# Optimization experiments

Measured on AMD Instinct MI355X. Metric: run time of the kernel, lower is better.

Reference implementation:

```python
import jax, jax.numpy as jnp
from jax import lax
import numpy as np

PI = np.float32(np.pi)
DN = ('NCHW', 'OIHW', 'NCHW')
PAD = [(1, 1), (1, 1)]


def setup_inputs() -> dict:
    key = jax.random.key(0)
    k1, k2 = jax.random.split(key, 2)
    B, C, H, W_ = 8, 64, 256, 256
    OUT, K = 64, 8
    x = jax.random.normal(k1, (B, C, H, W_), dtype=jnp.float32)
    # kaiming-normal-like scale for 3x3 conv weights
    W = jax.random.normal(k2, (K, OUT, C, 3, 3), dtype=jnp.float32) * np.float32(np.sqrt(2.0 / (C * 9)))
    b = jnp.zeros((K, OUT), dtype=jnp.float32)  # nn.init.zeros_(conv.bias)
    return {"x": x, "W": W, "b": b}


def reference(x, W, b):
    B, C, H, Wd = x.shape
    K = W.shape[0]
    sx = jnp.array([[1, 0, -1], [2, 0, -2], [1, 0, -1]], dtype=jnp.float32)
    sy = jnp.array([[1, 2, 1], [0, 0, 0], [-1, -2, -1]], dtype=jnp.float32)
    kx = jnp.tile(sx[None, None], (C, 1, 1, 1))  # (C,1,3,3) depthwise
    ky = jnp.tile(sy[None, None], (C, 1, 1, 1))
    grad_x = lax.conv_general_dilated(x, kx, (1, 1), PAD, dimension_numbers=DN, feature_group_count=C)
    grad_y = lax.conv_general_dilated(x, ky, (1, 1), PAD, dimension_numbers=DN, feature_group_count=C)
    theta = jnp.arctan2(grad_y, grad_x)
    # ((theta+pi)/(2pi)*K).long() % K ; values >= 0 so trunc == floor
    q = ((theta + PI) / (2 * PI) * K).astype(jnp.int32) % K  # (B,C,H,W)
    out = jnp.zeros((B, W.shape[1], H, Wd), dtype=x.dtype)
    for k in range(K):
        mask = (q == k).astype(x.dtype)
        fk = lax.conv_general_dilated(x * mask, W[k], (1, 1), PAD, dimension_numbers=DN)
        out = out + fk + b[k][None, :, None, None]
    return out / K
```

## Files before the change

kernel.cpp:

```cpp
#include <hip/hip_runtime.h>
#include <math.h>


#define TH 16
#define TW 32

typedef __attribute__((ext_vector_type(8)))  short    short8;
typedef __attribute__((ext_vector_type(16))) float    f32x16;
typedef __attribute__((ext_vector_type(4)))  unsigned u32x4;

__device__ __forceinline__ float atanf_fdlibm(float x) {
#pragma clang fp contract(off)
    const float atanhi0 = 4.6364760399e-01f, atanhi1 = 7.8539812565e-01f,
                atanhi2 = 9.8279368877e-01f, atanhi3 = 1.5707962513e+00f;
    const float atanlo0 = 5.0121582440e-09f, atanlo1 = 3.7748947079e-08f,
                atanlo2 = 3.4473217170e-08f, atanlo3 = 7.5497894159e-08f;
    const float aT0 = 3.3333334327e-01f, aT1 = -2.0000000298e-01f, aT2 = 1.4285714924e-01f,
                aT3 = -1.1111110449e-01f, aT4 = 9.0908870101e-02f, aT5 = -7.6918758452e-02f,
                aT6 = 6.6610731184e-02f, aT7 = -5.8335702866e-02f, aT8 = 4.9768779427e-02f,
                aT9 = -3.6531571299e-02f, aT10 = 1.6285819933e-02f;

    int hx = __float_as_int(x);
    int ix = hx & 0x7fffffff;
    int id;
    if (ix >= 0x4c800000) {
        if (ix > 0x7f800000) return x + x;
        return (hx > 0) ? (atanhi3 + atanlo3) : (-atanhi3 - atanlo3);
    }
    if (ix < 0x3ee00000) {
        if (ix < 0x31000000) return x;
        id = -1;
    } else {
        x = fabsf(x);
        if (ix < 0x3f980000) {
            if (ix < 0x3f300000) { id = 0; x = (2.0f * x - 1.0f) / (2.0f + x); }
            else                 { id = 1; x = (x - 1.0f) / (x + 1.0f); }
        } else {
            if (ix < 0x401c0000) { id = 2; x = (x - 1.5f) / (1.0f + 1.5f * x); }
            else                 { id = 3; x = -1.0f / x; }
        }
    }
    float z = x * x;
    float w = z * z;
    float s1 = z * (aT0 + w * (aT2 + w * (aT4 + w * (aT6 + w * (aT8 + w * aT10)))));
    float s2 = w * (aT1 + w * (aT3 + w * (aT5 + w * (aT7 + w * aT9))));
    if (id < 0) return x - x * (s1 + s2);
    float r;
    if      (id == 0) r = atanhi0 - ((x * (s1 + s2) - atanlo0) - x);
    else if (id == 1) r = atanhi1 - ((x * (s1 + s2) - atanlo1) - x);
    else if (id == 2) r = atanhi2 - ((x * (s1 + s2) - atanlo2) - x);
    else              r = atanhi3 - ((x * (s1 + s2) - atanlo3) - x);
    return (hx < 0) ? -r : r;
}

__device__ __forceinline__ float atan2f_fdlibm(float y, float x) {
#pragma clang fp contract(off)
    const float tiny = 1.0e-30f;
    const float pi_o_4 = 7.8539818525e-01f;
    const float pi_o_2 = 1.5707963705e+00f;
    const float pi     = 3.1415927410e+00f;
    const float pi_lo  = -8.7422776573e-08f;

    int hx = __float_as_int(x), hy = __float_as_int(y);
    int ix = hx & 0x7fffffff, iy = hy & 0x7fffffff;
    if (ix > 0x7f800000 || iy > 0x7f800000) return x + y;
    if (hx == 0x3f800000) return atanf_fdlibm(y);
    int m = ((hy >> 31) & 1) | ((hx >> 30) & 2);

    if (iy == 0) {
        switch (m) {
            case 0:
            case 1:  return y;
            case 2:  return  pi + tiny;
            default: return -pi - tiny;
        }
    }
    if (ix == 0) return (hy < 0) ? (-pi_o_2 - tiny) : (pi_o_2 + tiny);
    if (ix == 0x7f800000) {
        if (iy == 0x7f800000) {
            switch (m) {
                case 0:  return  pi_o_4 + tiny;
                case 1:  return -pi_o_4 - tiny;
                case 2:  return  3.0f * pi_o_4 + tiny;
                default: return -3.0f * pi_o_4 - tiny;
            }
        } else {
            switch (m) {
                case 0:  return  0.0f;
                case 1:  return -0.0f;
                case 2:  return  pi + tiny;
                default: return -pi - tiny;
            }
        }
    }
    if (iy == 0x7f800000) return (hy < 0) ? (-pi_o_2 - tiny) : (pi_o_2 + tiny);

    int k = (iy - ix) >> 23;
    float z;
    int mm = m;
    if (k > 26)                    { z = pi_o_2 + 0.5f * pi_lo; mm &= 1; }
    else if (hx < 0 && k < -26)    { z = 0.0f; }
    else                           { z = atanf_fdlibm(fabsf(y / x)); }

    switch (mm) {
        case 0:  return z;
        case 1:  return -z;
        case 2:  return pi - (z - pi_lo);
        default: return (z - pi_lo) - pi;
    }
}

__device__ __forceinline__ int bin8(float gy, float gx) {
#pragma clang fp contract(off)
    float th = atan2f_fdlibm(gy, gx);
    float t  = th + 3.14159274101257324f;
    float u  = t / 6.28318548202514648f;
    u = u * 8.0f;
    return ((int)u) & 7;
}

__device__ __forceinline__ unsigned rne_bf16_bits(float f) {
    unsigned u = __float_as_uint(f);
    return (u + 0x7fffu + ((u >> 16) & 1u)) >> 16;
}

__global__ __launch_bounds__(256)
void bin_kernel(const float* __restrict__ x, unsigned* __restrict__ pwg) {
    __shared__ float rs[3][260];
    const int w    = threadIdx.x;
    const int hrow = blockIdx.x;
    const int img  = blockIdx.y;
    const float* xim = x + ((size_t)img << 16);
    #pragma unroll
    for (int r = 0; r < 3; ++r) {
        int gh = hrow - 1 + r;
        float v = 0.f;
        if ((unsigned)gh < 256u) v = xim[(gh << 8) + w];
        rs[r][w + 1] = v;
        if (w == 0) { rs[r][0] = 0.f; rs[r][257] = 0.f; }
    }
    __syncthreads();
    int q; unsigned hv;
    {
#pragma clang fp contract(off)
        float a0 = rs[0][w], a1 = rs[0][w + 1], a2 = rs[0][w + 2];
        float m0 = rs[1][w],                    m2 = rs[1][w + 2];
        float z0 = rs[2][w], z1 = rs[2][w + 1], z2 = rs[2][w + 2];
        float gx = ((((a0 - a2) + 2.0f * m0) - 2.0f * m2) + z0) - z2;
        float gy = ((((a0 + 2.0f * a1) + a2) - z0) - 2.0f * z1) - z2;
        q  = bin8(gy, gx);
        hv = rne_bf16_bits(rs[1][w + 1]);
    }
    pwg[((size_t)img << 16) + (hrow << 8) + w] = (hv << 16) | (unsigned)q;
}

__global__ void prep_w2(const float* __restrict__ Wg, short* __restrict__ wsw) {
    int tid = blockIdx.x * 256 + threadIdx.x;
    if (tid >= 4096) return;
    int c = tid >> 6, o = tid & 63;
    for (int t = 0; t < 9; ++t)
        #pragma unroll
        for (int k = 0; k < 8; ++k)
            wsw[((((c * 10 + t) << 6) + o) << 3) + k] =
                (short)rne_bf16_bits(Wg[(((k << 6) + o) * 64 + c) * 9 + t]);
    #pragma unroll
    for (int k = 0; k < 8; ++k)
        wsw[((((c * 10 + 9) << 6) + o) << 3) + k] = 0;
}

__device__ __forceinline__ void build_oh(unsigned pv, u32x4* dst) {
    unsigned q  = pv & 7u;
    unsigned hv = (q & 1u) ? (pv & 0xffff0000u) : (pv >> 16);
    unsigned s2 = q >> 1;
    u32x4 oh;
    oh.x = (s2 == 0u) ? hv : 0u;
    oh.y = (s2 == 1u) ? hv : 0u;
    oh.z = (s2 == 2u) ? hv : 0u;
    oh.w = (s2 == 3u) ? hv : 0u;
    *dst = oh;
}

__global__ __launch_bounds__(256, 2)
void dirconv_mfma2(const unsigned* __restrict__ pwg,
                   const short*    __restrict__ wsw,
                   const float*    __restrict__ bg,
                   float*          __restrict__ out) {
    __shared__ u32x4 pwx[2][648];
    __shared__ u32x4 wl2[2][640];
    __shared__ float bsum[64];

    const int tid  = threadIdx.x;
    const int wave = tid >> 6;
    const int lane = tid & 63;
    const int h    = lane >> 5;
    const int l31  = lane & 31;
    const int bb   = blockIdx.z;
    const int h0   = blockIdx.y * TH;
    const int w0c  = blockIdx.x * TW;

    if (tid < 64) {
        float s = 0.f;
        #pragma unroll
        for (int k = 0; k < 8; ++k) s += bg[k * 64 + tid];
        bsum[tid] = s;
    }

    f32x16 acc[2][4];
    #pragma unroll
    for (int i = 0; i < 2; ++i)
        #pragma unroll
        for (int j = 0; j < 4; ++j)
            acc[i][j] = (f32x16)0.f;

    int rro[5], c2o[5];
    #pragma unroll
    for (int s = 0; s < 5; ++s) {
        int t = 2 * s + h;
        int t3 = t / 3;
        rro[s] = (t <= 8) ? t3 : 0;
        c2o[s] = (t <= 8) ? (t - t3 * 3) : 0;
    }

    {
        const u32x4* wsrc = (const u32x4*)wsw;
        wl2[0][tid]       = wsrc[tid];
        wl2[0][tid + 256] = wsrc[tid + 256];
        if (tid < 128) wl2[0][tid + 512] = wsrc[tid + 512];
        const unsigned* pimg = pwg + ((size_t)(bb * 64) << 16);
        #pragma unroll
        for (int rd = 0; rd < 3; ++rd) {
            int idx = tid + rd * 256;
            if (idx < 612) {
                int r = idx / 34, cc2 = idx - r * 34;
                int gh = h0 + r - 1, gw = w0c + cc2 - 1;
                unsigned pv = 0;
                if ((unsigned)gh < 256u && (unsigned)gw < 256u)
                    pv = pimg[(gh << 8) + gw];
                build_oh(pv, &pwx[0][r * 36 + cc2]);
            }
        }
    }
    __syncthreads();

    #pragma unroll 2
    for (int c = 0; c < 64; ++c) {
        const int cb = c & 1, nb = cb ^ 1;
        u32x4 wv0 = (u32x4)0u, wv1 = (u32x4)0u, wv2 = (u32x4)0u;
        unsigned pv0 = 0, pv1 = 0, pv2 = 0;

        if (c < 63) {
            const u32x4* wsrc = (const u32x4*)(wsw + (size_t)(c + 1) * 5120);
            wv0 = wsrc[tid];
            wv1 = wsrc[tid + 256];
            if (tid < 128) wv2 = wsrc[tid + 512];
            const unsigned* pimg = pwg + ((size_t)(bb * 64 + c + 1) << 16);
            {   int idx = tid;       int r = idx / 34, cc2 = idx - r * 34;
                int gh = h0 + r - 1, gw = w0c + cc2 - 1;
                if ((unsigned)gh < 256u && (unsigned)gw < 256u) pv0 = pimg[(gh << 8) + gw]; }
            {   int idx = tid + 256; int r = idx / 34, cc2 = idx - r * 34;
                int gh = h0 + r - 1, gw = w0c + cc2 - 1;
                if ((unsigned)gh < 256u && (unsigned)gw < 256u) pv1 = pimg[(gh << 8) + gw]; }
            if (tid < 100) {
                int idx = tid + 512; int r = idx / 34, cc2 = idx - r * 34;
                int gh = h0 + r - 1, gw = w0c + cc2 - 1;
                if ((unsigned)gh < 256u && (unsigned)gw < 256u) pv2 = pimg[(gh << 8) + gw]; }
        }

        {
            const u32x4* pb = &pwx[cb][0];
            const u32x4* wb = &wl2[cb][0];
            #pragma unroll
            for (int s = 0; s < 5; ++s) {
                const int t = 2 * s + h;
                short8 a0 = __builtin_bit_cast(short8, wb[t * 64 + l31]);
                short8 a1 = __builtin_bit_cast(short8, wb[t * 64 + 32 + l31]);
                #pragma unroll
                for (int nf = 0; nf < 4; ++nf) {
                    int py = wave * 4 + nf;
                    short8 bf = __builtin_bit_cast(short8,
                                    pb[(py + rro[s]) * 36 + l31 + c2o[s]]);
                    acc[0][nf] = __builtin_amdgcn_mfma_f32_32x32x16_bf16(a0, bf, acc[0][nf], 0, 0, 0);
                    acc[1][nf] = __builtin_amdgcn_mfma_f32_32x32x16_bf16(a1, bf, acc[1][nf], 0, 0, 0);
                }
            }
        }

        if (c < 63) {
            wl2[nb][tid]       = wv0;
            wl2[nb][tid + 256] = wv1;
            if (tid < 128) wl2[nb][tid + 512] = wv2;
            {   int idx = tid;       int r = idx / 34, cc2 = idx - r * 34;
                build_oh(pv0, &pwx[nb][r * 36 + cc2]); }
            {   int idx = tid + 256; int r = idx / 34, cc2 = idx - r * 34;
                build_oh(pv1, &pwx[nb][r * 36 + cc2]); }
            if (tid < 100) {
                int idx = tid + 512; int r = idx / 34, cc2 = idx - r * 34;
                build_oh(pv2, &pwx[nb][r * 36 + cc2]); }
        }
        __syncthreads();
    }

    float* ob = out + ((size_t)bb << 22);
    #pragma unroll
    for (int mf = 0; mf < 2; ++mf)
        #pragma unroll
        for (int nf = 0; nf < 4; ++nf) {
            int py = wave * 4 + nf;
            #pragma unroll
            for (int reg = 0; reg < 16; ++reg) {
                int o = mf * 32 + (reg & 3) + 8 * (reg >> 2) + 4 * h;
                ob[((size_t)o << 16) + ((h0 + py) << 8) + (w0c + l31)] =
                    (acc[mf][nf][reg] + bsum[o]) * 0.125f;
            }
        }
}

__global__ __launch_bounds__(256, 2)
void dirconv_fb(const float* __restrict__ x,
                const float* __restrict__ Wg,
                const float* __restrict__ bg,
                float* __restrict__ out) {
    __shared__ float    xs[20 * 37];
    __shared__ unsigned pw[18 * 36];
    __shared__ short    wl[64][128];
    __shared__ float    bsum[64];

    const int tid  = threadIdx.x;
    const int wave = tid >> 6;
    const int lane = tid & 63;
    const int h    = lane >> 5;
    const int l31  = lane & 31;
    const int bb   = blockIdx.z;
    const int h0   = blockIdx.y * TH;
    const int w0   = blockIdx.x * TW;

    if (tid < 64) {
        float s = 0.f;
        #pragma unroll
        for (int k = 0; k < 8; ++k) s += bg[k * 64 + tid];
        bsum[tid] = s;
    }

    f32x16 acc[2][4];
    #pragma unroll
    for (int i = 0; i < 2; ++i)
        #pragma unroll
        for (int j = 0; j < 4; ++j)
            acc[i][j] = (f32x16)0.f;

    const int swz0 = l31 & 7;

    for (int c = 0; c < 64; ++c) {
        __syncthreads();
        const float* xc = x + ((size_t)(bb * 64 + c) << 16);
        for (int idx = tid; idx < 720; idx += 256) {
            int r = idx / 36, cc = idx - r * 36;
            int gh = h0 + r - 2, gw = w0 + cc - 2;
            float v = 0.f;
            if ((unsigned)gh < 256u && (unsigned)gw < 256u)
                v = xc[(gh << 8) + gw];
            xs[r * 37 + cc] = v;
        }
        for (int pair = tid; pair < 512; pair += 256) {
            int k = pair >> 6, o = pair & 63;
            const float* g = Wg + ((size_t)((k << 6) + o) * 64 + c) * 9;
            #pragma unroll
            for (int t = 0; t < 9; ++t)
                wl[o][((t ^ (o & 7)) << 3) + k] = (short)rne_bf16_bits(g[t]);
        }
        if (tid < 64) {
            int o = tid;
            #pragma unroll
            for (int e = 0; e < 8; ++e) wl[o][((9 ^ (o & 7)) << 3) + e] = 0;
        }
        __syncthreads();

        for (int idx = tid; idx < 612; idx += 256) {
            int r = idx / 34, cc = idx - r * 34;
            const float* p0 = &xs[r * 37 + cc];
            int q; unsigned hv;
            {
#pragma clang fp contract(off)
                float a0 = p0[0],  a1 = p0[1],  a2 = p0[2];
                float m0 = p0[37],              m2 = p0[39];
                float z0 = p0[74], z1 = p0[75], z2 = p0[76];
                float gx = ((((a0 - a2) + 2.0f * m0) - 2.0f * m2) + z0) - z2;
                float gy = ((((a0 + 2.0f * a1) + a2) - z0) - 2.0f * z1) - z2;
                q  = bin8(gy, gx);
                hv = rne_bf16_bits(p0[38]);
            }
            pw[r * 36 + cc] = (hv << 16) | (unsigned)q;
        }
        __syncthreads();

        #pragma unroll
        for (int s = 0; s < 5; ++s) {
            const int t = 2 * s + h;
            short8 a0 = *(const short8*)&wl[l31     ][(t ^ swz0) << 3];
            short8 a1 = *(const short8*)&wl[32 + l31][(t ^ swz0) << 3];
            const int t3 = t / 3;
            const int dy = t3 - 1, dx = t - t3 * 3 - 1;
            const bool val = (t <= 8);
            #pragma unroll
            for (int nf = 0; nf < 4; ++nf) {
                int py = wave * 4 + nf;
                int rr = val ? (py + 1 + dy) : 0;
                int c2 = val ? (l31 + 1 + dx) : 0;
                unsigned pv = pw[rr * 36 + c2];
                pv = val ? pv : 0u;
                unsigned q   = pv & 7u;
                unsigned hhi = pv & 0xffff0000u;
                unsigned hlo = pv >> 16;
                u32x4 bw;
                bw.x = (q == 0u ? hlo : 0u) | (q == 1u ? hhi : 0u);
                bw.y = (q == 2u ? hlo : 0u) | (q == 3u ? hhi : 0u);
                bw.z = (q == 4u ? hlo : 0u) | (q == 5u ? hhi : 0u);
                bw.w = (q == 6u ? hlo : 0u) | (q == 7u ? hhi : 0u);
                short8 bf = __builtin_bit_cast(short8, bw);
                acc[0][nf] = __builtin_amdgcn_mfma_f32_32x32x16_bf16(a0, bf, acc[0][nf], 0, 0, 0);
                acc[1][nf] = __builtin_amdgcn_mfma_f32_32x32x16_bf16(a1, bf, acc[1][nf], 0, 0, 0);
            }
        }
    }

    float* ob = out + ((size_t)bb << 22);
    #pragma unroll
    for (int mf = 0; mf < 2; ++mf)
        #pragma unroll
        for (int nf = 0; nf < 4; ++nf) {
            int py = wave * 4 + nf;
            #pragma unroll
            for (int reg = 0; reg < 16; ++reg) {
                int o = mf * 32 + (reg & 3) + 8 * (reg >> 2) + 4 * h;
                ob[((size_t)o << 16) + ((h0 + py) << 8) + (w0 + l31)] =
                    (acc[mf][nf][reg] + bsum[o]) * 0.125f;
            }
        }
}

extern "C" void kernel_launch(void* const* d_in, const int* in_sizes, int n_in,
                              void* d_out, int out_size, void* d_ws, size_t ws_size,
                              hipStream_t stream) {
    const float* x  = (const float*)d_in[0];
    const float* Wg = (const float*)d_in[1];
    const float* bg = (const float*)d_in[2];
    float* out = (float*)d_out;

    dim3 grid(256 / TW, 256 / TH, 8);
    dim3 block(256);

    const size_t pw_bytes   = (size_t)8 * 64 * 256 * 256 * 4;
    const size_t wsw2_bytes = (size_t)64 * 10 * 64 * 8 * 2;

    if (ws_size >= pw_bytes + wsw2_bytes) {
        unsigned* pwg = (unsigned*)d_ws;
        short*    wsw = (short*)((char*)d_ws + pw_bytes);
        bin_kernel<<<dim3(256, 512, 1), 256, 0, stream>>>(x, pwg);
        prep_w2<<<16, 256, 0, stream>>>(Wg, wsw);
        dirconv_mfma2<<<grid, block, 0, stream>>>(pwg, wsw, bg, out);
    } else {
        dirconv_fb<<<grid, block, 0, stream>>>(x, Wg, bg, out);
    }
}
```

Baseline: 445.7 us.

## Interleave LDS staging writes with MFMA steps and branch-free atan2 binning

The main conv loop now interleaves the next channel's weight and one-hot LDS writes between the five MFMA steps, raising wave priority around each MFMA group with s_setprio, so LDS stores overlap matrix work instead of following it. The unroll-2 pragma is removed. Separately, the binning kernel replaces the branchy fdlibm atan2 with a select-based version that evaluates all range-reduction cases, to avoid warp divergence. The branchless atan2 must reproduce the exact bin edges of the original. The loop restructuring may shift register pressure or scheduling.

```diff
diff --git a/kernel.cpp b/kernel.cpp
--- a/kernel.cpp
+++ b/kernel.cpp
@@ -119,6 +119,69 @@
     return ((int)u) & 7;
 }
 
+__device__ __forceinline__ int bin8_bf(float gy, float gx) {
+#pragma clang fp contract(off)
+    const float aT0 = 3.3333334327e-01f, aT1 = -2.0000000298e-01f, aT2 = 1.4285714924e-01f,
+                aT3 = -1.1111110449e-01f, aT4 = 9.0908870101e-02f, aT5 = -7.6918758452e-02f,
+                aT6 = 6.6610731184e-02f, aT7 = -5.8335702866e-02f, aT8 = 4.9768779427e-02f,
+                aT9 = -3.6531571299e-02f, aT10 = 1.6285819933e-02f;
+    const float pi    = 3.1415927410e+00f;
+    const float pi_lo = -8.7422776573e-08f;
+    const float pio2  = 1.5707963705e+00f;
+
+    int hx = __float_as_int(gx), hy = __float_as_int(gy);
+    int ix = hx & 0x7fffffff,   iy = hy & 0x7fffffff;
+    int m  = ((hy >> 31) & 1) | ((hx >> 30) & 2);
+
+    float q  = fabsf(gy / gx);
+    int   iq = __float_as_int(q);
+
+    bool lt04375 = iq < 0x3ee00000;
+    bool lt06875 = iq < 0x3f300000;
+    bool lt11875 = iq < 0x3f980000;
+    bool lt24375 = iq < 0x401c0000;
+
+    float n0 = 2.0f * q - 1.0f, d0 = 2.0f + q;
+    float n1 = q - 1.0f,        d1 = q + 1.0f;
+    float n2 = q - 1.5f,        d2 = 1.0f + 1.5f * q;
+    float num = lt04375 ? q    : lt06875 ? n0 : lt11875 ? n1 : lt24375 ? n2 : -1.0f;
+    float den = lt04375 ? 1.0f : lt06875 ? d0 : lt11875 ? d1 : lt24375 ? d2 : q;
+    float hi  = lt06875 ? 4.6364760399e-01f : lt11875 ? 7.8539812565e-01f
+              : lt24375 ? 9.8279368877e-01f : 1.5707962513e+00f;
+    float lo  = lt06875 ? 5.0121582440e-09f : lt11875 ? 3.7748947079e-08f
+              : lt24375 ? 3.4473217170e-08f : 7.5497894159e-08f;
+
+    float a  = num / den;
+    float z2 = a * a;
+    float w2 = z2 * z2;
+    float s1 = z2 * (aT0 + w2 * (aT2 + w2 * (aT4 + w2 * (aT6 + w2 * (aT8 + w2 * aT10)))));
+    float s2 = w2 * (aT1 + w2 * (aT3 + w2 * (aT5 + w2 * (aT7 + w2 * aT9))));
+    float S  = s1 + s2;
+    float resm1 = a - a * S;
+    float resid = hi - ((a * S - lo) - a);
+    float zr = lt04375 ? resm1 : resid;
+    zr = (iq >= 0x4c800000) ? (1.5707962513e+00f + 7.5497894159e-08f) : zr;
+
+    int  k    = (iy - ix) >> 23;
+    bool kbig = k > 26;
+    float z   = kbig ? (pio2 + 0.5f * pi_lo) : zr;
+    z = (hx < 0 && k < -26) ? 0.0f : z;
+    int mm = kbig ? (m & 1) : m;
+
+    float w  = z - pi_lo;
+    float r2 = pi - w;
+    float r3 = w - pi;
+    float res = (mm == 0) ? z : (mm == 1) ? -z : (mm == 2) ? r2 : r3;
+    res = (ix == 0) ? ((hy < 0) ? -pio2 : pio2) : res;
+    float piy = (m == 2) ? pi : (m == 3) ? -pi : gy;
+    res = (iy == 0) ? piy : res;
+
+    float t = res + 3.14159274101257324f;
+    float u = t / 6.28318548202514648f;
+    u = u * 8.0f;
+    return ((int)u) & 7;
+}
+
 __device__ __forceinline__ unsigned rne_bf16_bits(float f) {
     unsigned u = __float_as_uint(f);
     return (u + 0x7fffu + ((u >> 16) & 1u)) >> 16;
@@ -148,7 +211,7 @@
         float z0 = rs[2][w], z1 = rs[2][w + 1], z2 = rs[2][w + 2];
         float gx = ((((a0 - a2) + 2.0f * m0) - 2.0f * m2) + z0) - z2;
         float gy = ((((a0 + 2.0f * a1) + a2) - z0) - 2.0f * z1) - z2;
-        q  = bin8(gy, gx);
+        q  = bin8_bf(gy, gx);
         hv = rne_bf16_bits(rs[1][w + 1]);
     }
     pwg[((size_t)img << 16) + (hrow << 8) + w] = (hv << 16) | (unsigned)q;
@@ -242,13 +305,13 @@
     }
     __syncthreads();
 
-    #pragma unroll 2
     for (int c = 0; c < 64; ++c) {
         const int cb = c & 1, nb = cb ^ 1;
         u32x4 wv0 = (u32x4)0u, wv1 = (u32x4)0u, wv2 = (u32x4)0u;
         unsigned pv0 = 0, pv1 = 0, pv2 = 0;
-
-        if (c < 63) {
+        const bool more = (c < 63);
+
+        if (more) {
             const u32x4* wsrc = (const u32x4*)(wsw + (size_t)(c + 1) * 5120);
             wv0 = wsrc[tid];
             wv1 = wsrc[tid + 256];
@@ -266,37 +329,50 @@
                 if ((unsigned)gh < 256u && (unsigned)gw < 256u) pv2 = pimg[(gh << 8) + gw]; }
         }
 
-        {
-            const u32x4* pb = &pwx[cb][0];
-            const u32x4* wb = &wl2[cb][0];
+        const u32x4* pb = &pwx[cb][0];
+        const u32x4* wb = &wl2[cb][0];
+        auto mfma_step = [&](int s) {
+            const int t = 2 * s + h;
+            short8 a0 = __builtin_bit_cast(short8, wb[t * 64 + l31]);
+            short8 a1 = __builtin_bit_cast(short8, wb[t * 64 + 32 + l31]);
             #pragma unroll
-            for (int s = 0; s < 5; ++s) {
-                const int t = 2 * s + h;
-                short8 a0 = __builtin_bit_cast(short8, wb[t * 64 + l31]);
-                short8 a1 = __builtin_bit_cast(short8, wb[t * 64 + 32 + l31]);
-                #pragma unroll
-                for (int nf = 0; nf < 4; ++nf) {
-                    int py = wave * 4 + nf;
-                    short8 bf = __builtin_bit_cast(short8,
-                                    pb[(py + rro[s]) * 36 + l31 + c2o[s]]);
-                    acc[0][nf] = __builtin_amdgcn_mfma_f32_32x32x16_bf16(a0, bf, acc[0][nf], 0, 0, 0);
-                    acc[1][nf] = __builtin_amdgcn_mfma_f32_32x32x16_bf16(a1, bf, acc[1][nf], 0, 0, 0);
-                }
-            }
-        }
-
-        if (c < 63) {
+            for (int nf = 0; nf < 4; ++nf) {
+                int py = wave * 4 + nf;
+                short8 bf = __builtin_bit_cast(short8,
+                                pb[(py + rro[s]) * 36 + l31 + c2o[s]]);
+                acc[0][nf] = __builtin_amdgcn_mfma_f32_32x32x16_bf16(a0, bf, acc[0][nf], 0, 0, 0);
+                acc[1][nf] = __builtin_amdgcn_mfma_f32_32x32x16_bf16(a1, bf, acc[1][nf], 0, 0, 0);
+            }
+        };
+
+        __builtin_amdgcn_s_setprio(1);
+        mfma_step(0);
+        mfma_step(1);
+        __builtin_amdgcn_s_setprio(0);
+        if (more) {
             wl2[nb][tid]       = wv0;
             wl2[nb][tid + 256] = wv1;
             if (tid < 128) wl2[nb][tid + 512] = wv2;
+        }
+        __builtin_amdgcn_s_setprio(1);
+        mfma_step(2);
+        __builtin_amdgcn_s_setprio(0);
+        if (more) {
             {   int idx = tid;       int r = idx / 34, cc2 = idx - r * 34;
                 build_oh(pv0, &pwx[nb][r * 36 + cc2]); }
             {   int idx = tid + 256; int r = idx / 34, cc2 = idx - r * 34;
                 build_oh(pv1, &pwx[nb][r * 36 + cc2]); }
-            if (tid < 100) {
-                int idx = tid + 512; int r = idx / 34, cc2 = idx - r * 34;
-                build_oh(pv2, &pwx[nb][r * 36 + cc2]); }
-        }
+        }
+        __builtin_amdgcn_s_setprio(1);
+        mfma_step(3);
+        __builtin_amdgcn_s_setprio(0);
+        if (more && tid < 100) {
+            int idx = tid + 512; int r = idx / 34, cc2 = idx - r * 34;
+            build_oh(pv2, &pwx[nb][r * 36 + cc2]);
+        }
+        __builtin_amdgcn_s_setprio(1);
+        mfma_step(4);
+        __builtin_amdgcn_s_setprio(0);
         __syncthreads();
     }
 
```

Result: faster. 416.0 us (-6.7%).
